# Optimization experiments

Hardware: AMD Instinct MI355X
Metric: run time of the kernel (lower is better)

The kernel has to match this reference:

```python
import jax, jax.numpy as jnp
import numpy as np

B, TQ, TK, DK, DV = 64, 1024, 1024, 64, 64


def setup_inputs() -> dict:
    key = jax.random.key(0)
    kq, kk, kv, km = jax.random.split(key, 4)
    q = jax.random.normal(kq, (B, TQ, DK), dtype=jnp.float32)
    k = jax.random.normal(kk, (B, TK, DK), dtype=jnp.float32)
    v = jax.random.normal(kv, (B, TK, DV), dtype=jnp.float32)
    mask = jax.random.randint(km, (B, TQ, TK), 0, 2).astype(jnp.int32)
    return {"q": q, "k": k, "v": v, "mask": mask}


def reference(q, k, v, mask):
    # attn = q @ k^T / sqrt(d_k)   -> [B, TQ, TK]
    temper = jnp.sqrt(jnp.asarray(q.shape[-1], dtype=jnp.float32))
    attn = jnp.einsum('bqd,bkd->bqk', q, k) / temper
    # mask-add: -1e9 where mask == 0
    mmask = -1e9 * (1.0 - mask.astype(jnp.float32))
    attn = attn + mmask
    attn = jax.nn.softmax(attn, axis=-1)
    # dropout rate is 0.0 -> identity
    out = jnp.einsum('bqk,bkd->bqd', attn, v)
    return (out, attn)
```

## Files before the change

kernel.cpp:

```cpp
#include <hip/hip_runtime.h>
#include <hip/hip_bf16.h>


#define B_   64
#define TQ_  1024
#define TK_  1024
#define DD   64

typedef short short8 __attribute__((ext_vector_type(8)));
typedef float f32x4 __attribute__((ext_vector_type(4)));

#define PSTR 264
#define VSTR 40
#define PWAVE (16 * PSTR)
#define VWAVE (64 * VSTR)

__device__ __forceinline__ unsigned cvt2(float a, float b) {
    __hip_bfloat162 h = __float22bfloat162_rn(make_float2(a, b));
    unsigned u; __builtin_memcpy(&u, &h, 4); return u;
}
__device__ __forceinline__ short cvt1(float a) {
    __hip_bfloat16 h = __float2bfloat16(a);
    short s; __builtin_memcpy(&s, &h, 2); return s;
}

union Frag { short8 s; unsigned u[4]; };

__global__ __launch_bounds__(256, 3) void attn_mfma_kernel(
    const float* __restrict__ qg, const float* __restrict__ kg,
    const float* __restrict__ vg, const int* __restrict__ maskg,
    float* __restrict__ outg, float* __restrict__ attng)
{
    __shared__ __align__(16) short p_lds[4 * PWAVE];
    __shared__ __align__(16) short vt_lds[4 * VWAVE];

    const int t    = threadIdx.x;
    const int wave = t >> 6, lane = t & 63;
    const int quad = lane >> 4, n16 = lane & 15;
    const int b    = blockIdx.y;
    const int q0   = blockIdx.x * 16;
    const int kbase = wave * 256;

    short* pw = p_lds + wave * PWAVE;
    short* vw = vt_lds + wave * VWAVE;
    float* redmax = (float*)vt_lds;
    float* redsum = (float*)vt_lds + 64;

    Frag aq[2];
    {
        const float* qp = qg + ((size_t)(b * TQ_ + q0 + n16)) * DD + quad * 8;
        #pragma unroll
        for (int f = 0; f < 2; ++f) {
            float4 x = *(const float4*)(qp + f * 32);
            float4 y = *(const float4*)(qp + f * 32 + 4);
            aq[f].u[0] = cvt2(x.x, x.y); aq[f].u[1] = cvt2(x.z, x.w);
            aq[f].u[2] = cvt2(y.x, y.y); aq[f].u[3] = cvt2(y.z, y.w);
        }
    }

    float s_reg[64];

    const float* kbp = kg + (size_t)b * TK_ * DD;
    const int*   mbp = maskg + ((size_t)(b * TQ_ + q0 + quad * 4)) * TK_ + kbase + n16;
    #pragma unroll
    for (int kt = 0; kt < 16; ++kt) {
        const int key0 = kbase + kt * 16;
        const float* kp = kbp + (size_t)(key0 + n16) * DD + quad * 8;
        Frag bk[2];
        #pragma unroll
        for (int f = 0; f < 2; ++f) {
            float4 x = *(const float4*)(kp + f * 32);
            float4 y = *(const float4*)(kp + f * 32 + 4);
            bk[f].u[0] = cvt2(x.x, x.y); bk[f].u[1] = cvt2(x.z, x.w);
            bk[f].u[2] = cvt2(y.x, y.y); bk[f].u[3] = cvt2(y.z, y.w);
        }
        f32x4 acc = {0.f, 0.f, 0.f, 0.f};
        acc = __builtin_amdgcn_mfma_f32_16x16x32_bf16(aq[0].s, bk[0].s, acc, 0, 0, 0);
        acc = __builtin_amdgcn_mfma_f32_16x16x32_bf16(aq[1].s, bk[1].s, acc, 0, 0, 0);
        #pragma unroll
        for (int r = 0; r < 4; ++r) {
            const int m = mbp[(size_t)r * TK_ + kt * 16];
            s_reg[kt * 4 + r] = acc[r] * 0.125f + (m ? 0.f : -1e9f);
        }
    }

    float rmax[4];
    #pragma unroll
    for (int r = 0; r < 4; ++r) {
        float m = s_reg[r];
        #pragma unroll
        for (int kt = 1; kt < 16; ++kt) m = fmaxf(m, s_reg[kt * 4 + r]);
        #pragma unroll
        for (int off = 8; off > 0; off >>= 1) m = fmaxf(m, __shfl_xor(m, off));
        rmax[r] = m;
    }
    if (n16 == 0) {
        #pragma unroll
        for (int r = 0; r < 4; ++r) redmax[wave * 16 + quad * 4 + r] = rmax[r];
    }
    __syncthreads();
    float gmax[4];
    #pragma unroll
    for (int r = 0; r < 4; ++r) {
        const int row = quad * 4 + r;
        gmax[r] = fmaxf(fmaxf(redmax[row], redmax[16 + row]),
                        fmaxf(redmax[32 + row], redmax[48 + row]));
    }
    float lsum[4] = {0.f, 0.f, 0.f, 0.f};
    #pragma unroll
    for (int kt = 0; kt < 16; ++kt) {
        #pragma unroll
        for (int r = 0; r < 4; ++r) {
            const float p = __expf(s_reg[kt * 4 + r] - gmax[r]);
            s_reg[kt * 4 + r] = p;
            lsum[r] += p;
        }
    }
    #pragma unroll
    for (int r = 0; r < 4; ++r) {
        #pragma unroll
        for (int off = 8; off > 0; off >>= 1) lsum[r] += __shfl_xor(lsum[r], off);
    }
    if (n16 == 0) {
        #pragma unroll
        for (int r = 0; r < 4; ++r) redsum[wave * 16 + quad * 4 + r] = lsum[r];
    }
    __syncthreads();
    float inv[4];
    #pragma unroll
    for (int r = 0; r < 4; ++r) {
        const int row = quad * 4 + r;
        inv[r] = 1.f / (redsum[row] + redsum[16 + row] + redsum[32 + row] + redsum[48 + row]);
    }
    __syncthreads();

    float* abp = attng + ((size_t)(b * TQ_ + q0 + quad * 4)) * TK_ + kbase + n16;
    #pragma unroll
    for (int kt = 0; kt < 16; ++kt) {
        #pragma unroll
        for (int r = 0; r < 4; ++r) {
            const float pv = s_reg[kt * 4 + r] * inv[r];
            abp[(size_t)r * TK_ + kt * 16] = pv;
            pw[(quad * 4 + r) * PSTR + kt * 16 + n16] = cvt1(pv);
        }
    }

    f32x4 oacc[4];
    #pragma unroll
    for (int dg = 0; dg < 4; ++dg) oacc[dg] = (f32x4){0.f, 0.f, 0.f, 0.f};

    const float* vbp = vg + (size_t)b * TK_ * DD;
    #pragma unroll 1
    for (int c = 0; c < 8; ++c) {
        const int ck0 = kbase + c * 32;
        #pragma unroll
        for (int i = 0; i < 16; ++i) {
            const float v0 = vbp[(size_t)(ck0 + 2 * i) * DD + lane];
            const float v1 = vbp[(size_t)(ck0 + 2 * i + 1) * DD + lane];
            *(unsigned*)(vw + lane * VSTR + 2 * i) = cvt2(v0, v1);
        }
        Frag pf;
        pf.s = *(const short8*)(pw + n16 * PSTR + c * 32 + quad * 8);
        #pragma unroll
        for (int dg = 0; dg < 4; ++dg) {
            Frag vf;
            vf.s = *(const short8*)(vw + (dg * 16 + n16) * VSTR + quad * 8);
            oacc[dg] = __builtin_amdgcn_mfma_f32_16x16x32_bf16(pf.s, vf.s, oacc[dg], 0, 0, 0);
        }
    }

    float* ow = (float*)pw;
    #pragma unroll
    for (int dg = 0; dg < 4; ++dg) {
        #pragma unroll
        for (int r = 0; r < 4; ++r)
            ow[(quad * 4 + r) * 68 + dg * 16 + n16] = oacc[dg][r];
    }
    __syncthreads();
    {
        const int row = t >> 4;
        const int col = (t & 15) * 4;
        const float* p0 = (const float*)p_lds;
        float4 o = make_float4(0.f, 0.f, 0.f, 0.f);
        #pragma unroll
        for (int w = 0; w < 4; ++w) {
            const float4 x = *(const float4*)(p0 + w * (PWAVE / 2) + row * 68 + col);
            o.x += x.x; o.y += x.y; o.z += x.z; o.w += x.w;
        }
        *(float4*)(outg + ((size_t)(b * TQ_ + q0 + row)) * DD + col) = o;
    }
}

extern "C" void kernel_launch(void* const* d_in, const int* in_sizes, int n_in,
                              void* d_out, int out_size, void* d_ws, size_t ws_size,
                              hipStream_t stream) {
    const float* q    = (const float*)d_in[0];
    const float* k    = (const float*)d_in[1];
    const float* v    = (const float*)d_in[2];
    const int*   mask = (const int*)d_in[3];

    float* out  = (float*)d_out;
    float* attn = out + (size_t)B_ * TQ_ * DD;

    dim3 grid(TQ_ / 16, B_);
    attn_mfma_kernel<<<grid, 256, 0, stream>>>(q, k, v, mask, out, attn);
}
```

Measured before the change: 630.7 us.

## Transpose MFMA operands for row-contiguous mask/attn I/O and prefetch V in registers

Swaps MFMA operand order so each lane owns four consecutive keys of one query row. Mask loads and attention stores become int4/float4 vectors, and the row max and sum need only two cross-lane shuffles. The 1/sqrt(d) scale is folded into Q before the bf16 conversion. V chunks are software-prefetched into registers one chunk ahead, and P is staged to LDS in two halves to shrink shared memory and allow 4 blocks per CU. The cost is more live registers under a tighter launch bound, and scaling Q before rounding can shift bf16 results slightly.

```diff
diff --git a/kernel.cpp b/kernel.cpp
--- a/kernel.cpp
+++ b/kernel.cpp
@@ -10,29 +10,26 @@
 typedef short short8 __attribute__((ext_vector_type(8)));
 typedef float f32x4 __attribute__((ext_vector_type(4)));
 
-#define PSTR 264
-#define VSTR 40
-#define PWAVE (16 * PSTR)
-#define VWAVE (64 * VSTR)
+#define PLW    68
+#define PL_U32 (16 * PLW)
+#define VSTR   40
+#define VT_SH  (64 * VSTR)
+#define WVS    (2 * PL_U32 + VT_SH)
 
 __device__ __forceinline__ unsigned cvt2(float a, float b) {
     __hip_bfloat162 h = __float22bfloat162_rn(make_float2(a, b));
     unsigned u; __builtin_memcpy(&u, &h, 4); return u;
 }
-__device__ __forceinline__ short cvt1(float a) {
-    __hip_bfloat16 h = __float2bfloat16(a);
-    short s; __builtin_memcpy(&s, &h, 2); return s;
-}
 
 union Frag { short8 s; unsigned u[4]; };
 
-__global__ __launch_bounds__(256, 3) void attn_mfma_kernel(
+__global__ __launch_bounds__(256, 4) void attn_mfma_kernel(
     const float* __restrict__ qg, const float* __restrict__ kg,
     const float* __restrict__ vg, const int* __restrict__ maskg,
     float* __restrict__ outg, float* __restrict__ attng)
 {
-    __shared__ __align__(16) short p_lds[4 * PWAVE];
-    __shared__ __align__(16) short vt_lds[4 * VWAVE];
+    __shared__ __align__(16) short lds[4 * WVS];
+    __shared__ float red[128];
 
     const int t    = threadIdx.x;
     const int wave = t >> 6, lane = t & 63;
@@ -41,10 +38,9 @@
     const int q0   = blockIdx.x * 16;
     const int kbase = wave * 256;
 
-    short* pw = p_lds + wave * PWAVE;
-    short* vw = vt_lds + wave * VWAVE;
-    float* redmax = (float*)vt_lds;
-    float* redsum = (float*)vt_lds + 64;
+    short*    wbase = lds + wave * WVS;
+    unsigned* pl    = (unsigned*)wbase;
+    short*    vw    = wbase + 2 * PL_U32;
 
     Frag aq[2];
     {
@@ -53,19 +49,20 @@
         for (int f = 0; f < 2; ++f) {
             float4 x = *(const float4*)(qp + f * 32);
             float4 y = *(const float4*)(qp + f * 32 + 4);
-            aq[f].u[0] = cvt2(x.x, x.y); aq[f].u[1] = cvt2(x.z, x.w);
-            aq[f].u[2] = cvt2(y.x, y.y); aq[f].u[3] = cvt2(y.z, y.w);
+            aq[f].u[0] = cvt2(0.125f * x.x, 0.125f * x.y);
+            aq[f].u[1] = cvt2(0.125f * x.z, 0.125f * x.w);
+            aq[f].u[2] = cvt2(0.125f * y.x, 0.125f * y.y);
+            aq[f].u[3] = cvt2(0.125f * y.z, 0.125f * y.w);
         }
     }
 
     float s_reg[64];
 
-    const float* kbp = kg + (size_t)b * TK_ * DD;
-    const int*   mbp = maskg + ((size_t)(b * TQ_ + q0 + quad * 4)) * TK_ + kbase + n16;
+    const float* kbp  = kg + (size_t)b * TK_ * DD;
+    const int*   mrow = maskg + ((size_t)(b * TQ_ + q0 + n16)) * TK_ + kbase + quad * 4;
     #pragma unroll
     for (int kt = 0; kt < 16; ++kt) {
-        const int key0 = kbase + kt * 16;
-        const float* kp = kbp + (size_t)(key0 + n16) * DD + quad * 8;
+        const float* kp = kbp + (size_t)(kbase + kt * 16 + n16) * DD + quad * 8;
         Frag bk[2];
         #pragma unroll
         for (int f = 0; f < 2; ++f) {
@@ -74,117 +71,146 @@
             bk[f].u[0] = cvt2(x.x, x.y); bk[f].u[1] = cvt2(x.z, x.w);
             bk[f].u[2] = cvt2(y.x, y.y); bk[f].u[3] = cvt2(y.z, y.w);
         }
+        const int4 mk = *(const int4*)(mrow + kt * 16);
         f32x4 acc = {0.f, 0.f, 0.f, 0.f};
-        acc = __builtin_amdgcn_mfma_f32_16x16x32_bf16(aq[0].s, bk[0].s, acc, 0, 0, 0);
-        acc = __builtin_amdgcn_mfma_f32_16x16x32_bf16(aq[1].s, bk[1].s, acc, 0, 0, 0);
-        #pragma unroll
-        for (int r = 0; r < 4; ++r) {
-            const int m = mbp[(size_t)r * TK_ + kt * 16];
-            s_reg[kt * 4 + r] = acc[r] * 0.125f + (m ? 0.f : -1e9f);
-        }
-    }
-
-    float rmax[4];
-    #pragma unroll
-    for (int r = 0; r < 4; ++r) {
-        float m = s_reg[r];
-        #pragma unroll
-        for (int kt = 1; kt < 16; ++kt) m = fmaxf(m, s_reg[kt * 4 + r]);
-        #pragma unroll
-        for (int off = 8; off > 0; off >>= 1) m = fmaxf(m, __shfl_xor(m, off));
-        rmax[r] = m;
-    }
-    if (n16 == 0) {
-        #pragma unroll
-        for (int r = 0; r < 4; ++r) redmax[wave * 16 + quad * 4 + r] = rmax[r];
-    }
+        acc = __builtin_amdgcn_mfma_f32_16x16x32_bf16(bk[0].s, aq[0].s, acc, 0, 0, 0);
+        acc = __builtin_amdgcn_mfma_f32_16x16x32_bf16(bk[1].s, aq[1].s, acc, 0, 0, 0);
+        s_reg[kt * 4 + 0] = acc[0] + (mk.x ? 0.f : -1e9f);
+        s_reg[kt * 4 + 1] = acc[1] + (mk.y ? 0.f : -1e9f);
+        s_reg[kt * 4 + 2] = acc[2] + (mk.z ? 0.f : -1e9f);
+        s_reg[kt * 4 + 3] = acc[3] + (mk.w ? 0.f : -1e9f);
+    }
+
+    const float* vbp = vg + (size_t)b * TK_ * DD;
+    unsigned va16[16];
+    #pragma unroll
+    for (int i = 0; i < 16; ++i) {
+        const float v0 = vbp[(size_t)(kbase + 2 * i) * DD + lane];
+        const float v1 = vbp[(size_t)(kbase + 2 * i + 1) * DD + lane];
+        va16[i] = cvt2(v0, v1);
+    }
+
+    float m8[8];
+    #pragma unroll
+    for (int j = 0; j < 8; ++j) m8[j] = s_reg[j];
+    #pragma unroll
+    for (int i = 8; i < 64; i += 8)
+        #pragma unroll
+        for (int j = 0; j < 8; ++j) m8[j] = fmaxf(m8[j], s_reg[i + j]);
+    float m = fmaxf(fmaxf(fmaxf(m8[0], m8[1]), fmaxf(m8[2], m8[3])),
+                    fmaxf(fmaxf(m8[4], m8[5]), fmaxf(m8[6], m8[7])));
+    m = fmaxf(m, __shfl_xor(m, 16));
+    m = fmaxf(m, __shfl_xor(m, 32));
+    if (lane < 16) red[wave * 16 + n16] = m;
     __syncthreads();
-    float gmax[4];
-    #pragma unroll
-    for (int r = 0; r < 4; ++r) {
-        const int row = quad * 4 + r;
-        gmax[r] = fmaxf(fmaxf(redmax[row], redmax[16 + row]),
-                        fmaxf(redmax[32 + row], redmax[48 + row]));
-    }
-    float lsum[4] = {0.f, 0.f, 0.f, 0.f};
-    #pragma unroll
-    for (int kt = 0; kt < 16; ++kt) {
-        #pragma unroll
-        for (int r = 0; r < 4; ++r) {
-            const float p = __expf(s_reg[kt * 4 + r] - gmax[r]);
-            s_reg[kt * 4 + r] = p;
-            lsum[r] += p;
-        }
-    }
-    #pragma unroll
-    for (int r = 0; r < 4; ++r) {
-        #pragma unroll
-        for (int off = 8; off > 0; off >>= 1) lsum[r] += __shfl_xor(lsum[r], off);
-    }
-    if (n16 == 0) {
-        #pragma unroll
-        for (int r = 0; r < 4; ++r) redsum[wave * 16 + quad * 4 + r] = lsum[r];
-    }
+    const float gm = fmaxf(fmaxf(red[n16], red[16 + n16]),
+                           fmaxf(red[32 + n16], red[48 + n16]));
+    float l0 = 0.f, l1 = 0.f, l2 = 0.f, l3 = 0.f;
+    #pragma unroll
+    for (int i = 0; i < 16; ++i) {
+        const float p0 = __expf(s_reg[4*i+0] - gm);
+        const float p1 = __expf(s_reg[4*i+1] - gm);
+        const float p2 = __expf(s_reg[4*i+2] - gm);
+        const float p3 = __expf(s_reg[4*i+3] - gm);
+        s_reg[4*i+0] = p0; s_reg[4*i+1] = p1;
+        s_reg[4*i+2] = p2; s_reg[4*i+3] = p3;
+        l0 += p0; l1 += p1; l2 += p2; l3 += p3;
+    }
+    float lsum = (l0 + l1) + (l2 + l3);
+    lsum += __shfl_xor(lsum, 16);
+    lsum += __shfl_xor(lsum, 32);
+    if (lane < 16) red[64 + wave * 16 + n16] = lsum;
     __syncthreads();
-    float inv[4];
-    #pragma unroll
-    for (int r = 0; r < 4; ++r) {
-        const int row = quad * 4 + r;
-        inv[r] = 1.f / (redsum[row] + redsum[16 + row] + redsum[32 + row] + redsum[48 + row]);
-    }
-    __syncthreads();
-
-    float* abp = attng + ((size_t)(b * TQ_ + q0 + quad * 4)) * TK_ + kbase + n16;
-    #pragma unroll
-    for (int kt = 0; kt < 16; ++kt) {
-        #pragma unroll
-        for (int r = 0; r < 4; ++r) {
-            const float pv = s_reg[kt * 4 + r] * inv[r];
-            abp[(size_t)r * TK_ + kt * 16] = pv;
-            pw[(quad * 4 + r) * PSTR + kt * 16 + n16] = cvt1(pv);
-        }
+    const float inv = 1.f / (red[64 + n16] + red[80 + n16] +
+                             red[96 + n16] + red[112 + n16]);
+    #pragma unroll
+    for (int i = 0; i < 64; ++i) s_reg[i] *= inv;
+
+    float* ab = attng + ((size_t)(b * TQ_ + q0 + n16)) * TK_ + kbase + quad * 4;
+    #pragma unroll
+    for (int kt = 0; kt < 16; ++kt)
+        *(float4*)(ab + kt * 16) = make_float4(s_reg[kt*4+0], s_reg[kt*4+1],
+                                               s_reg[kt*4+2], s_reg[kt*4+3]);
+    #pragma unroll
+    for (int kt = 0; kt < 8; ++kt) {
+        uint2 u;
+        u.x = cvt2(s_reg[kt*4+0], s_reg[kt*4+1]);
+        u.y = cvt2(s_reg[kt*4+2], s_reg[kt*4+3]);
+        *(uint2*)&pl[n16 * PLW + kt * 8 + quad * 2] = u;
     }
 
     f32x4 oacc[4];
     #pragma unroll
     for (int dg = 0; dg < 4; ++dg) oacc[dg] = (f32x4){0.f, 0.f, 0.f, 0.f};
 
-    const float* vbp = vg + (size_t)b * TK_ * DD;
     #pragma unroll 1
-    for (int c = 0; c < 8; ++c) {
-        const int ck0 = kbase + c * 32;
-        #pragma unroll
-        for (int i = 0; i < 16; ++i) {
-            const float v0 = vbp[(size_t)(ck0 + 2 * i) * DD + lane];
-            const float v1 = vbp[(size_t)(ck0 + 2 * i + 1) * DD + lane];
-            *(unsigned*)(vw + lane * VSTR + 2 * i) = cvt2(v0, v1);
+    for (int c = 0; c < 4; ++c) {
+        #pragma unroll
+        for (int i = 0; i < 16; ++i)
+            *(unsigned*)(vw + lane * VSTR + 2 * i) = va16[i];
+        {
+            const int ck = kbase + (c + 1) * 32;
+            #pragma unroll
+            for (int i = 0; i < 16; ++i) {
+                const float v0 = vbp[(size_t)(ck + 2 * i) * DD + lane];
+                const float v1 = vbp[(size_t)(ck + 2 * i + 1) * DD + lane];
+                va16[i] = cvt2(v0, v1);
+            }
         }
         Frag pf;
-        pf.s = *(const short8*)(pw + n16 * PSTR + c * 32 + quad * 8);
+        pf.s = *(const short8*)&pl[n16 * PLW + c * 16 + quad * 4];
         #pragma unroll
         for (int dg = 0; dg < 4; ++dg) {
             Frag vf;
             vf.s = *(const short8*)(vw + (dg * 16 + n16) * VSTR + quad * 8);
-            oacc[dg] = __builtin_amdgcn_mfma_f32_16x16x32_bf16(pf.s, vf.s, oacc[dg], 0, 0, 0);
-        }
-    }
-
-    float* ow = (float*)pw;
-    #pragma unroll
-    for (int dg = 0; dg < 4; ++dg) {
-        #pragma unroll
-        for (int r = 0; r < 4; ++r)
-            ow[(quad * 4 + r) * 68 + dg * 16 + n16] = oacc[dg][r];
-    }
+            oacc[dg] = __builtin_amdgcn_mfma_f32_16x16x32_bf16(vf.s, pf.s, oacc[dg], 0, 0, 0);
+        }
+    }
+
+    #pragma unroll
+    for (int kt = 8; kt < 16; ++kt) {
+        uint2 u;
+        u.x = cvt2(s_reg[kt*4+0], s_reg[kt*4+1]);
+        u.y = cvt2(s_reg[kt*4+2], s_reg[kt*4+3]);
+        *(uint2*)&pl[n16 * PLW + (kt - 8) * 8 + quad * 2] = u;
+    }
+
+    #pragma unroll 1
+    for (int c = 0; c < 4; ++c) {
+        #pragma unroll
+        for (int i = 0; i < 16; ++i)
+            *(unsigned*)(vw + lane * VSTR + 2 * i) = va16[i];
+        if (c < 3) {
+            const int ck = kbase + (c + 5) * 32;
+            #pragma unroll
+            for (int i = 0; i < 16; ++i) {
+                const float v0 = vbp[(size_t)(ck + 2 * i) * DD + lane];
+                const float v1 = vbp[(size_t)(ck + 2 * i + 1) * DD + lane];
+                va16[i] = cvt2(v0, v1);
+            }
+        }
+        Frag pf;
+        pf.s = *(const short8*)&pl[n16 * PLW + c * 16 + quad * 4];
+        #pragma unroll
+        for (int dg = 0; dg < 4; ++dg) {
+            Frag vf;
+            vf.s = *(const short8*)(vw + (dg * 16 + n16) * VSTR + quad * 8);
+            oacc[dg] = __builtin_amdgcn_mfma_f32_16x16x32_bf16(vf.s, pf.s, oacc[dg], 0, 0, 0);
+        }
+    }
+
+    float* ow = (float*)pl;
+    #pragma unroll
+    for (int dg = 0; dg < 4; ++dg)
+        *(f32x4*)&ow[n16 * PLW + dg * 16 + quad * 4] = oacc[dg];
     __syncthreads();
     {
-        const int row = t >> 4;
-        const int col = (t & 15) * 4;
-        const float* p0 = (const float*)p_lds;
+        const int row = t >> 4, col = (t & 15) * 4;
+        const float* base = (const float*)lds;
         float4 o = make_float4(0.f, 0.f, 0.f, 0.f);
         #pragma unroll
         for (int w = 0; w < 4; ++w) {
-            const float4 x = *(const float4*)(p0 + w * (PWAVE / 2) + row * 68 + col);
+            const float4 x = *(const float4*)(base + w * (WVS / 2) + row * PLW + col);
             o.x += x.x; o.y += x.y; o.z += x.z; o.w += x.w;
         }
         *(float4*)(outg + ((size_t)(b * TQ_ + q0 + row)) * DD + col) = o;
```

After: 653.5 us. 1.04x slower.
